# Performance work log

Hardware: AMD Instinct MI355X
Metric: run time of the kernel (lower is better)

The kernel has to match this reference:

```python
import jax, jax.numpy as jnp
import numpy as np

B, H, W, N = 8, 192, 192, 1000
DOWN_H = DOWN_W = 8.0
MIN_RADIUS = 8.0
COUNT_WEIGHT, SCALE_WEIGHT, SPATIAL_WEIGHT = 2.0, 0.5, 0.1
EPS = 1e-8


def setup_inputs() -> dict:
    key = jax.random.key(0)
    k1, k2 = jax.random.split(key)
    # non-negative density map (like a sigmoid/relu head output)
    dens = jax.random.uniform(k1, (B, 1, H, W), dtype=jnp.float32) * 0.5
    scale = jnp.array([W * DOWN_W, H * DOWN_H], dtype=jnp.float32)
    points = jax.random.uniform(k2, (B, N, 2), dtype=jnp.float32) * scale
    return {"dens": dens, "points": points}


def reference(dens, points):
    cell_area = DOWN_H * DOWN_W
    # grid cell centers in input-image coordinates
    yy = jnp.arange(H, dtype=jnp.float32)[:, None] * DOWN_H + DOWN_H / 2  # [H,1]
    xx = jnp.arange(W, dtype=jnp.float32)[None, :] * DOWN_W + DOWN_W / 2  # [1,W]

    pred = dens[:, 0]                                   # [B,H,W]
    gt_count = jnp.float32(N)
    pred_count = jnp.sum(pred, axis=(1, 2)) / cell_area  # [B]
    count_loss = jnp.abs(pred_count - gt_count)          # [B]
    scale_loss = count_loss / gt_count                   # [B] (gt_count > 0)

    def spatial_one(args):
        p, pts = args  # p: [H,W], pts: [N,2]
        # squared distance from every grid center to every point: [N,H,W]
        d2 = (xx[None] - pts[:, 0, None, None]) ** 2 + (yy[None] - pts[:, 1, None, None]) ** 2
        min_dist = jnp.sqrt(jnp.min(d2, axis=0))  # min of sqrt == sqrt of min
        target = jax.nn.sigmoid((MIN_RADIUS - min_dist) / (MIN_RADIUS * 0.5))
        pm, tm = jnp.max(p), jnp.max(target)
        pn = p / jnp.maximum(pm, EPS)
        tn = target / jnp.maximum(tm, EPS)
        mse = jnp.mean((pn - tn) ** 2)
        return jnp.where((pm > EPS) & (tm > EPS), mse, jnp.float32(0.0))

    # sequential over batch to bound the [N,H,W] intermediate (mirrors the torch per-image loop)
    spatial_loss = jax.lax.map(spatial_one, (pred, points))  # [B]

    total = (COUNT_WEIGHT * jnp.mean(count_loss)
             + SCALE_WEIGHT * jnp.mean(scale_loss)
             + SPATIAL_WEIGHT * jnp.mean(spatial_loss))
    return total
```

## Files before the change

### kernel.cpp

```cpp
#include <hip/hip_runtime.h>
#include <math.h>

#define NB 8
#define NH 192
#define NW 192
#define NPTS 1000
#define TW 32
#define TH 12
#define NPIX (TW * TH)

constexpr float KDOWN = 8.0f;


__global__ __launch_bounds__(256) void heavy(const float* __restrict__ dens,
                                             const float* __restrict__ points,
                                             float* __restrict__ parts) {
  __shared__ float4 kept[NPTS];
  __shared__ float d2all[4][NPIX];
  __shared__ float wmin[4];
  __shared__ float sred[4][6];
  __shared__ int scnt;

  const int b = blockIdx.z;
  const int col0 = blockIdx.x * TW;
  const int row0 = blockIdx.y * TH;
  const float cx = (float)col0 * KDOWN + 128.0f;
  const float cy = (float)row0 * KDOWN + 48.0f;
  const int tid = threadIdx.x;
  const int lane = tid & 63;
  const int w = tid >> 6;

  const int prow = tid >> 5;
  const int pcol = tid & 31;
  float pred0 = dens[((size_t)b * NH + row0 + prow) * NW + col0 + pcol];
  float pred1 = 0.0f;
  if (tid < 128)
    pred1 = dens[((size_t)b * NH + row0 + 8 + prow) * NW + col0 + pcol];

  if (tid == 0) scnt = 0;

  const float2* __restrict__ pb =
      reinterpret_cast<const float2*>(points) + (size_t)b * NPTS;

  float2 P0[4];
#pragma unroll
  for (int r = 0; r < 4; ++r) {
    int j = r * 256 + tid;
    P0[r] = (j < NPTS) ? pb[j] : make_float2(1.0e19f, 1.0e19f);
  }
  float qmin = 3.0e38f;
#pragma unroll
  for (int r = 0; r < 4; ++r) {
    int j = r * 256 + tid;
    if (j < NPTS) {
      float px = P0[r].x - cx, py = P0[r].y - cy;
      qmin = fminf(qmin, __builtin_fmaf(px, px, py * py));
    }
  }
#pragma unroll
  for (int off = 32; off > 0; off >>= 1)
    qmin = fminf(qmin, __shfl_down(qmin, off));
  if (lane == 0) wmin[w] = qmin;
  __syncthreads();

  const float M2 = fminf(fminf(wmin[0], wmin[1]), fminf(wmin[2], wmin[3]));
  const float thr = sqrtf(M2) + 2.0f * 131.58f + 1.0f;
  const float T = thr * thr;

#pragma unroll
  for (int r = 0; r < 4; ++r) {
    int j = r * 256 + tid;
    bool keep = false;
    float px = 0.f, py = 0.f, q = 0.f;
    if (j < NPTS) {
      px = P0[r].x - cx;
      py = P0[r].y - cy;
      q = __builtin_fmaf(px, px, py * py);
      keep = (q <= T);
    }
    unsigned long long mask = __ballot(keep);
    int base = 0;
    if (lane == 0) base = atomicAdd(&scnt, __popcll(mask));
    base = __shfl(base, 0);
    if (keep) {
      int pos = base + __popcll(mask & ((1ull << lane) - 1ull));
      kept[pos] = make_float4(px, py, q, 0.0f);
    }
  }
  __syncthreads();
  const int cnt = scnt;

  const int c = lane & 31;
  const int half = lane >> 5;
  const float xt = (float)(col0 + c) * KDOWN + 4.0f - cx;
  const float mx = -2.0f * xt;
  float my[6], xy2[6], d2[6];
#pragma unroll
  for (int k = 0; k < 6; ++k) {
    float ytk = (float)(row0 + half * 6 + k) * KDOWN + 4.0f - cy;
    my[k] = -2.0f * ytk;
    xy2[k] = __builtin_fmaf(xt, xt, ytk * ytk);
    d2[k] = 3.0e38f;
  }

  if (cnt > w) {
    const int M = (cnt - w + 3) >> 2;
    auto IDX = [&](int m) { m = (m < M) ? m : (M - 1); return w + 4 * m; };
    float4 A0 = kept[IDX(0)], A1 = kept[IDX(1)], A2 = kept[IDX(2)],
           A3 = kept[IDX(3)];
    for (int i0 = 0; i0 < M; i0 += 4) {
      float4 B0 = kept[IDX(i0 + 4)], B1 = kept[IDX(i0 + 5)],
             B2 = kept[IDX(i0 + 6)], B3 = kept[IDX(i0 + 7)];
#pragma unroll
      for (int k = 0; k < 6; ++k) {
        float t0 = __builtin_fmaf(my[k], A0.y, A0.z);
        t0 = __builtin_fmaf(mx, A0.x, t0);
        float t1 = __builtin_fmaf(my[k], A1.y, A1.z);
        t1 = __builtin_fmaf(mx, A1.x, t1);
        float t2 = __builtin_fmaf(my[k], A2.y, A2.z);
        t2 = __builtin_fmaf(mx, A2.x, t2);
        float t3 = __builtin_fmaf(my[k], A3.y, A3.z);
        t3 = __builtin_fmaf(mx, A3.x, t3);
        d2[k] = fminf(d2[k], fminf(fminf(t0, t1), fminf(t2, t3)));
      }
      A0 = B0; A1 = B1; A2 = B2; A3 = B3;
    }
  }

#pragma unroll
  for (int k = 0; k < 6; ++k)
    d2all[w][(half * 6 + k) * TW + c] = d2[k] + xy2[k];
  __syncthreads();

  float sp = 0.f, spp = 0.f, spt = 0.f, stt = 0.f, mp = 0.f, mt = 0.f;
  {
    int p = tid;
    float m4 = fminf(fminf(d2all[0][p], d2all[1][p]),
                     fminf(d2all[2][p], d2all[3][p]));
    float dd = fmaxf(m4, 0.0f);
    float md = sqrtf(dd);
    float x = (8.0f - md) * 0.25f;
    float tg = 1.0f / (1.0f + __expf(-x));
    sp += pred0;
    spp = __builtin_fmaf(pred0, pred0, spp);
    spt = __builtin_fmaf(pred0, tg, spt);
    stt = __builtin_fmaf(tg, tg, stt);
    mp = fmaxf(mp, pred0);
    mt = fmaxf(mt, tg);
  }
  if (tid < 128) {
    int p = tid + 256;
    float m4 = fminf(fminf(d2all[0][p], d2all[1][p]),
                     fminf(d2all[2][p], d2all[3][p]));
    float dd = fmaxf(m4, 0.0f);
    float md = sqrtf(dd);
    float x = (8.0f - md) * 0.25f;
    float tg = 1.0f / (1.0f + __expf(-x));
    sp += pred1;
    spp = __builtin_fmaf(pred1, pred1, spp);
    spt = __builtin_fmaf(pred1, tg, spt);
    stt = __builtin_fmaf(tg, tg, stt);
    mp = fmaxf(mp, pred1);
    mt = fmaxf(mt, tg);
  }

#pragma unroll
  for (int off = 32; off > 0; off >>= 1) {
    sp += __shfl_down(sp, off);
    spp += __shfl_down(spp, off);
    spt += __shfl_down(spt, off);
    stt += __shfl_down(stt, off);
    mp = fmaxf(mp, __shfl_down(mp, off));
    mt = fmaxf(mt, __shfl_down(mt, off));
  }
  if (lane == 0) {
    sred[w][0] = sp; sred[w][1] = spp; sred[w][2] = spt;
    sred[w][3] = stt; sred[w][4] = mp; sred[w][5] = mt;
  }
  __syncthreads();
  if (tid == 0) {
    const int bid =
        blockIdx.x + gridDim.x * (blockIdx.y + gridDim.y * blockIdx.z);
    float o[6];
#pragma unroll
    for (int i = 0; i < 4; ++i)
      o[i] = (sred[0][i] + sred[1][i]) + (sred[2][i] + sred[3][i]);
    o[4] = fmaxf(fmaxf(sred[0][4], sred[1][4]), fmaxf(sred[2][4], sred[3][4]));
    o[5] = fmaxf(fmaxf(sred[0][5], sred[1][5]), fmaxf(sred[2][5], sred[3][5]));
    float* dst = parts + (size_t)bid * 8;
#pragma unroll
    for (int i = 0; i < 6; ++i) dst[i] = o[i];
  }
}

__global__ __launch_bounds__(512) void finalize(const float* __restrict__ parts,
                                                float* __restrict__ out) {
  __shared__ double dres[8][3];
  const int tid = threadIdx.x;
  const int w = tid >> 6;
  const int lane = tid & 63;

  double sp = 0, spp = 0, spt = 0, stt = 0;
  float mp = 0.f, mt = 0.f;
  for (int e = lane; e < 96; e += 64) {
    const float* src = parts + (size_t)(w * 96 + e) * 8;
    sp += (double)src[0];
    spp += (double)src[1];
    spt += (double)src[2];
    stt += (double)src[3];
    mp = fmaxf(mp, src[4]);
    mt = fmaxf(mt, src[5]);
  }
#pragma unroll
  for (int off = 32; off > 0; off >>= 1) {
    sp += __shfl_down(sp, off);
    spp += __shfl_down(spp, off);
    spt += __shfl_down(spt, off);
    stt += __shfl_down(stt, off);
    mp = fmaxf(mp, __shfl_down(mp, off));
    mt = fmaxf(mt, __shfl_down(mt, off));
  }
  if (lane == 0) {
    double cl = fabs(sp / 64.0 - 1000.0);
    double pm = fmax((double)mp, 1e-8);
    double tm = fmax((double)mt, 1e-8);
    double mse =
        (spp / (pm * pm) - 2.0 * spt / (pm * tm) + stt / (tm * tm)) / 36864.0;
    double sps = (mp > 1e-8f && mt > 1e-8f) ? mse : 0.0;
    dres[w][0] = cl;
    dres[w][1] = cl / 1000.0;
    dres[w][2] = sps;
  }
  __syncthreads();
  if (tid == 0) {
    double cls = 0, sls = 0, sps = 0;
    for (int bb = 0; bb < 8; ++bb) {
      cls += dres[bb][0];
      sls += dres[bb][1];
      sps += dres[bb][2];
    }
    out[0] = (float)(2.0 * (cls / 8.0) + 0.5 * (sls / 8.0) + 0.1 * (sps / 8.0));
  }
}

extern "C" void kernel_launch(void* const* d_in, const int* in_sizes, int n_in,
                              void* d_out, int out_size, void* d_ws,
                              size_t ws_size, hipStream_t stream) {
  const float* dens = (const float*)d_in[0];
  const float* points = (const float*)d_in[1];
  float* parts = (float*)d_ws;
  float* out = (float*)d_out;

  dim3 grid(NW / TW, NH / TH, NB);
  hipLaunchKernelGGL(heavy, grid, dim3(256), 0, stream, dens, points, parts);
  hipLaunchKernelGGL(finalize, dim3(1), dim3(512), 0, stream, parts, out);
}
```

Measured before the change: 64.91 us.

## Use 512-thread blocks with per-wave local point compaction, removing shared atomic counter

The heavy kernel now runs 512 threads (8 waves) per tile, and each thread loads at most two points. Each wave compacts the points it keeps into its own shared list using ballot and popcount, so the block-wide atomic counter and one barrier are gone, and each wave scans only its own kept points. The eight per-wave minimum-distance buffers are then min-reduced per pixel. This doubles the parallelism applied to the point scan per tile and cuts synchronisation. In exchange it uses more shared memory per block, drops the software prefetch of point data, and leaves 128 idle threads in the final pixel pass.

```diff
diff --git a/kernel.cpp b/kernel.cpp
--- a/kernel.cpp
+++ b/kernel.cpp
@@ -12,14 +12,13 @@
 constexpr float KDOWN = 8.0f;
 
 
-__global__ __launch_bounds__(256) void heavy(const float* __restrict__ dens,
+__global__ __launch_bounds__(512) void heavy(const float* __restrict__ dens,
                                              const float* __restrict__ points,
                                              float* __restrict__ parts) {
-  __shared__ float4 kept[NPTS];
-  __shared__ float d2all[4][NPIX];
-  __shared__ float wmin[4];
-  __shared__ float sred[4][6];
-  __shared__ int scnt;
+  __shared__ float4 kept[8][128];
+  __shared__ float d2all[8][NPIX];
+  __shared__ float wmin[8];
+  __shared__ float sred[6][6];
 
   const int b = blockIdx.z;
   const int col0 = blockIdx.x * TW;
@@ -30,65 +29,44 @@
   const int lane = tid & 63;
   const int w = tid >> 6;
 
-  const int prow = tid >> 5;
-  const int pcol = tid & 31;
-  float pred0 = dens[((size_t)b * NH + row0 + prow) * NW + col0 + pcol];
-  float pred1 = 0.0f;
-  if (tid < 128)
-    pred1 = dens[((size_t)b * NH + row0 + 8 + prow) * NW + col0 + pcol];
-
-  if (tid == 0) scnt = 0;
+  float pred0 = 0.0f;
+  if (tid < NPIX)
+    pred0 = dens[((size_t)b * NH + row0 + (tid >> 5)) * NW + col0 + (tid & 31)];
 
   const float2* __restrict__ pb =
       reinterpret_cast<const float2*>(points) + (size_t)b * NPTS;
-
-  float2 P0[4];
-#pragma unroll
-  for (int r = 0; r < 4; ++r) {
-    int j = r * 256 + tid;
-    P0[r] = (j < NPTS) ? pb[j] : make_float2(1.0e19f, 1.0e19f);
-  }
-  float qmin = 3.0e38f;
-#pragma unroll
-  for (int r = 0; r < 4; ++r) {
-    int j = r * 256 + tid;
-    if (j < NPTS) {
-      float px = P0[r].x - cx, py = P0[r].y - cy;
-      qmin = fminf(qmin, __builtin_fmaf(px, px, py * py));
-    }
-  }
+  const int j0 = w * 64 + lane;
+  const int j1 = 512 + j0;
+  const bool v1 = (j1 < NPTS);
+  float2 P0 = pb[j0];
+  float2 P1 = v1 ? pb[j1] : make_float2(1.0e19f, 1.0e19f);
+  const float p0x = P0.x - cx, p0y = P0.y - cy;
+  const float p1x = P1.x - cx, p1y = P1.y - cy;
+  const float q0 = __builtin_fmaf(p0x, p0x, p0y * p0y);
+  const float q1 = __builtin_fmaf(p1x, p1x, p1y * p1y);
+
+  float qmin = fminf(q0, v1 ? q1 : 3.0e38f);
 #pragma unroll
   for (int off = 32; off > 0; off >>= 1)
     qmin = fminf(qmin, __shfl_down(qmin, off));
   if (lane == 0) wmin[w] = qmin;
   __syncthreads();
 
-  const float M2 = fminf(fminf(wmin[0], wmin[1]), fminf(wmin[2], wmin[3]));
+  float M2 = wmin[0];
+#pragma unroll
+  for (int i = 1; i < 8; ++i) M2 = fminf(M2, wmin[i]);
   const float thr = sqrtf(M2) + 2.0f * 131.58f + 1.0f;
   const float T = thr * thr;
 
-#pragma unroll
-  for (int r = 0; r < 4; ++r) {
-    int j = r * 256 + tid;
-    bool keep = false;
-    float px = 0.f, py = 0.f, q = 0.f;
-    if (j < NPTS) {
-      px = P0[r].x - cx;
-      py = P0[r].y - cy;
-      q = __builtin_fmaf(px, px, py * py);
-      keep = (q <= T);
-    }
-    unsigned long long mask = __ballot(keep);
-    int base = 0;
-    if (lane == 0) base = atomicAdd(&scnt, __popcll(mask));
-    base = __shfl(base, 0);
-    if (keep) {
-      int pos = base + __popcll(mask & ((1ull << lane) - 1ull));
-      kept[pos] = make_float4(px, py, q, 0.0f);
-    }
-  }
-  __syncthreads();
-  const int cnt = scnt;
+  const bool k0 = (q0 <= T);
+  const bool k1 = v1 && (q1 <= T);
+  const unsigned long long m0 = __ballot(k0);
+  const unsigned long long m1 = __ballot(k1);
+  const unsigned long long below = (lane == 63) ? ~0ull : ((1ull << (lane + 1)) - 1ull) >> 1;
+  if (k0) kept[w][__popcll(m0 & below)] = make_float4(p0x, p0y, q0, 0.0f);
+  if (k1) kept[w][__popcll(m0) + __popcll(m1 & below)] =
+      make_float4(p1x, p1y, q1, 0.0f);
+  const int M = __popcll(m0) + __popcll(m1);
 
   const int c = lane & 31;
   const int half = lane >> 5;
@@ -102,68 +80,47 @@
     xy2[k] = __builtin_fmaf(xt, xt, ytk * ytk);
     d2[k] = 3.0e38f;
   }
-
-  if (cnt > w) {
-    const int M = (cnt - w + 3) >> 2;
-    auto IDX = [&](int m) { m = (m < M) ? m : (M - 1); return w + 4 * m; };
-    float4 A0 = kept[IDX(0)], A1 = kept[IDX(1)], A2 = kept[IDX(2)],
-           A3 = kept[IDX(3)];
-    for (int i0 = 0; i0 < M; i0 += 4) {
-      float4 B0 = kept[IDX(i0 + 4)], B1 = kept[IDX(i0 + 5)],
-             B2 = kept[IDX(i0 + 6)], B3 = kept[IDX(i0 + 7)];
+  __builtin_amdgcn_wave_barrier();
+  asm volatile("s_waitcnt lgkmcnt(0)" ::: "memory");
+
+  const int Mc = (M > 0) ? M : 1;
+  if (M > 0) {
+    for (int i0 = 0; i0 < Mc; i0 += 4) {
+      int i1 = (i0 + 1 < Mc) ? i0 + 1 : Mc - 1;
+      int i2 = (i0 + 2 < Mc) ? i0 + 2 : Mc - 1;
+      int i3 = (i0 + 3 < Mc) ? i0 + 3 : Mc - 1;
+      float4 A0 = kept[w][i0], A1 = kept[w][i1], A2 = kept[w][i2],
+             A3 = kept[w][i3];
 #pragma unroll
       for (int k = 0; k < 6; ++k) {
-        float t0 = __builtin_fmaf(my[k], A0.y, A0.z);
-        t0 = __builtin_fmaf(mx, A0.x, t0);
-        float t1 = __builtin_fmaf(my[k], A1.y, A1.z);
-        t1 = __builtin_fmaf(mx, A1.x, t1);
-        float t2 = __builtin_fmaf(my[k], A2.y, A2.z);
-        t2 = __builtin_fmaf(mx, A2.x, t2);
-        float t3 = __builtin_fmaf(my[k], A3.y, A3.z);
-        t3 = __builtin_fmaf(mx, A3.x, t3);
+        float t0 = __builtin_fmaf(mx, A0.x, __builtin_fmaf(my[k], A0.y, A0.z));
+        float t1 = __builtin_fmaf(mx, A1.x, __builtin_fmaf(my[k], A1.y, A1.z));
+        float t2 = __builtin_fmaf(mx, A2.x, __builtin_fmaf(my[k], A2.y, A2.z));
+        float t3 = __builtin_fmaf(mx, A3.x, __builtin_fmaf(my[k], A3.y, A3.z));
         d2[k] = fminf(d2[k], fminf(fminf(t0, t1), fminf(t2, t3)));
       }
-      A0 = B0; A1 = B1; A2 = B2; A3 = B3;
     }
   }
-
 #pragma unroll
   for (int k = 0; k < 6; ++k)
     d2all[w][(half * 6 + k) * TW + c] = d2[k] + xy2[k];
   __syncthreads();
 
   float sp = 0.f, spp = 0.f, spt = 0.f, stt = 0.f, mp = 0.f, mt = 0.f;
-  {
-    int p = tid;
-    float m4 = fminf(fminf(d2all[0][p], d2all[1][p]),
-                     fminf(d2all[2][p], d2all[3][p]));
-    float dd = fmaxf(m4, 0.0f);
-    float md = sqrtf(dd);
+  if (tid < NPIX) {
+    float m8 = d2all[0][tid];
+#pragma unroll
+    for (int i = 1; i < 8; ++i) m8 = fminf(m8, d2all[i][tid]);
+    float md = sqrtf(fmaxf(m8, 0.0f));
     float x = (8.0f - md) * 0.25f;
     float tg = 1.0f / (1.0f + __expf(-x));
-    sp += pred0;
-    spp = __builtin_fmaf(pred0, pred0, spp);
-    spt = __builtin_fmaf(pred0, tg, spt);
-    stt = __builtin_fmaf(tg, tg, stt);
-    mp = fmaxf(mp, pred0);
-    mt = fmaxf(mt, tg);
-  }
-  if (tid < 128) {
-    int p = tid + 256;
-    float m4 = fminf(fminf(d2all[0][p], d2all[1][p]),
-                     fminf(d2all[2][p], d2all[3][p]));
-    float dd = fmaxf(m4, 0.0f);
-    float md = sqrtf(dd);
-    float x = (8.0f - md) * 0.25f;
-    float tg = 1.0f / (1.0f + __expf(-x));
-    sp += pred1;
-    spp = __builtin_fmaf(pred1, pred1, spp);
-    spt = __builtin_fmaf(pred1, tg, spt);
-    stt = __builtin_fmaf(tg, tg, stt);
-    mp = fmaxf(mp, pred1);
-    mt = fmaxf(mt, tg);
-  }
-
+    sp = pred0;
+    spp = pred0 * pred0;
+    spt = pred0 * tg;
+    stt = tg * tg;
+    mp = pred0;
+    mt = tg;
+  }
 #pragma unroll
   for (int off = 32; off > 0; off >>= 1) {
     sp += __shfl_down(sp, off);
@@ -173,20 +130,24 @@
     mp = fmaxf(mp, __shfl_down(mp, off));
     mt = fmaxf(mt, __shfl_down(mt, off));
   }
-  if (lane == 0) {
+  if (lane == 0 && w < 6) {
     sred[w][0] = sp; sred[w][1] = spp; sred[w][2] = spt;
     sred[w][3] = stt; sred[w][4] = mp; sred[w][5] = mt;
   }
   __syncthreads();
   if (tid == 0) {
-    const int bid =
-        blockIdx.x + gridDim.x * (blockIdx.y + gridDim.y * blockIdx.z);
     float o[6];
 #pragma unroll
     for (int i = 0; i < 4; ++i)
-      o[i] = (sred[0][i] + sred[1][i]) + (sred[2][i] + sred[3][i]);
-    o[4] = fmaxf(fmaxf(sred[0][4], sred[1][4]), fmaxf(sred[2][4], sred[3][4]));
-    o[5] = fmaxf(fmaxf(sred[0][5], sred[1][5]), fmaxf(sred[2][5], sred[3][5]));
+      o[i] = ((sred[0][i] + sred[1][i]) + (sred[2][i] + sred[3][i])) +
+             (sred[4][i] + sred[5][i]);
+    o[4] = fmaxf(fmaxf(fmaxf(sred[0][4], sred[1][4]),
+                       fmaxf(sred[2][4], sred[3][4])),
+                 fmaxf(sred[4][4], sred[5][4]));
+    o[5] = fmaxf(fmaxf(fmaxf(sred[0][5], sred[1][5]),
+                       fmaxf(sred[2][5], sred[3][5])),
+                 fmaxf(sred[4][5], sred[5][5]));
+    const int bid = b * 96 + blockIdx.y * gridDim.x + blockIdx.x;
     float* dst = parts + (size_t)bid * 8;
 #pragma unroll
     for (int i = 0; i < 6; ++i) dst[i] = o[i];
@@ -252,6 +213,6 @@
   float* out = (float*)d_out;
 
   dim3 grid(NW / TW, NH / TH, NB);
-  hipLaunchKernelGGL(heavy, grid, dim3(256), 0, stream, dens, points, parts);
+  hipLaunchKernelGGL(heavy, grid, dim3(512), 0, stream, dens, points, parts);
   hipLaunchKernelGGL(finalize, dim3(1), dim3(512), 0, stream, parts, out);
 }
```

Result: no change. 64.04 us (-1.3%).
